# Kernel tuning notes

Measured on AMD Instinct MI355X. Metric: run time of the kernel, lower is better.

The kernel has to match this reference:

```python
import jax, jax.numpy as jnp
import numpy as np

LN_EPS = 1e-5


def layernorm(x, g, b):
    mu = jnp.mean(x, axis=-1, keepdims=True)
    var = jnp.mean((x - mu) ** 2, axis=-1, keepdims=True)
    return (x - mu) * jax.lax.rsqrt(var + LN_EPS) * g + b


def attention(x, qkv_w, proj_w, proj_b, num_heads):
    B, N, C = x.shape
    d = C // num_heads
    qkv = jnp.einsum('bnc,oc->bno', x, qkv_w)            # [B,N,3C], no bias (qkv_bias=False)
    qkv = qkv.reshape(B, N, num_heads, 3 * d).transpose(0, 2, 1, 3)  # [B,h,N,3d]
    q, k, v = qkv[..., :d], qkv[..., d:2 * d], qkv[..., 2 * d:]
    scores = jnp.einsum('bhnd,bhmd->bhnm', q, k) * (d ** -0.5)
    a = jax.nn.softmax(scores, axis=-1)
    o = jnp.einsum('bhnm,bhmd->bhnd', a, v).transpose(0, 2, 1, 3).reshape(B, N, C)
    return jnp.einsum('bnc,oc->bno', o, proj_w) + proj_b


def dwconv(x, w, b, H, W):
    # x: [B,N,C] -> NCHW depthwise 3x3 conv, stride 1, pad 1 -> [B,N,C]
    B, N, C = x.shape
    xi = x.transpose(0, 2, 1).reshape(B, C, H, W)
    y = jax.lax.conv_general_dilated(
        xi, w, window_strides=(1, 1), padding='SAME',
        dimension_numbers=('NCHW', 'OIHW', 'NCHW'), feature_group_count=C)
    y = y + b[None, :, None, None]
    return y.reshape(B, C, H * W).transpose(0, 2, 1)


def mlp(x, fc1_w, fc1_b, dw_w, dw_b, fc2_w, fc2_b, H, W):
    h = jnp.einsum('bnc,oc->bno', x, fc1_w) + fc1_b
    h = dwconv(h, dw_w, dw_b, H, W)
    h = jax.nn.gelu(h, approximate=False)  # torch nn.GELU default = exact erf
    return jnp.einsum('bnh,oh->bno', h, fc2_w) + fc2_b


def setup_inputs() -> dict:
    key = jax.random.key(0)
    ks = jax.random.split(key, 8)
    B, N, C, HID = 8, 1024, 512, 2048
    s = 0.02
    return {
        'x': jax.random.normal(ks[0], (B, N, C), jnp.float32),
        'ln1_g': jnp.ones((C,), jnp.float32),
        'ln1_b': jnp.zeros((C,), jnp.float32),
        'qkv_w': jax.random.normal(ks[1], (3 * C, C), jnp.float32) * s,
        'proj_w': jax.random.normal(ks[2], (C, C), jnp.float32) * s,
        'proj_b': jnp.zeros((C,), jnp.float32),
        'ln2_g': jnp.ones((C,), jnp.float32),
        'ln2_b': jnp.zeros((C,), jnp.float32),
        'fc1_w': jax.random.normal(ks[3], (HID, C), jnp.float32) * s,
        'fc1_b': jnp.zeros((HID,), jnp.float32),
        'dw_w': jax.random.normal(ks[4], (HID, 1, 3, 3), jnp.float32) * s,
        'dw_b': jnp.zeros((HID,), jnp.float32),
        'fc2_w': jax.random.normal(ks[5], (C, HID), jnp.float32) * s,
        'fc2_b': jnp.zeros((C,), jnp.float32),
        'H': 32,
        'W': 32,
    }


def reference(x, ln1_g, ln1_b, qkv_w, proj_w, proj_b, ln2_g, ln2_b,
              fc1_w, fc1_b, dw_w, dw_b, fc2_w, fc2_b, H, W):
    NUM_HEADS = 8
    x = x + attention(layernorm(x, ln1_g, ln1_b), qkv_w, proj_w, proj_b, NUM_HEADS)
    x = x + mlp(layernorm(x, ln2_g, ln2_b), fc1_w, fc1_b, dw_w, dw_b, fc2_w, fc2_b, H, W)
    return x
```

## Files before the change

### kernel.cpp

```cpp
#include <hip/hip_runtime.h>
#include <hip/hip_bf16.h>


typedef __attribute__((ext_vector_type(8))) short short8;
typedef __attribute__((ext_vector_type(4))) short s16x4;
typedef __attribute__((ext_vector_type(4))) float f32x4;

__device__ __forceinline__ float b2f(short s) {
    union { float f; unsigned u; } z; z.u = ((unsigned)(unsigned short)s) << 16; return z.f;
}
__device__ __forceinline__ short f2b(float f) {
    union { float f; unsigned u; } z; z.f = f;
    unsigned r = (z.u + 0x7fffu + ((z.u >> 16) & 1u)) >> 16;
    return (short)r;
}
__device__ __forceinline__ float erf_fast(float x) {
    float ax = fabsf(x);
    float t = 1.0f / fmaf(0.3275911f, ax, 1.0f);
    float p = t * fmaf(t, fmaf(t, fmaf(t, fmaf(t, 1.061405429f, -1.453152027f),
                        1.421413741f), -0.284496736f), 0.254829592f);
    float r = 1.0f - p * __expf(-ax * ax);
    return x < 0.f ? -r : r;
}

__device__ __forceinline__ void gload_lds16(const void* g, void* l) {
    __builtin_amdgcn_global_load_lds(
        (const __attribute__((address_space(1))) void*)g,
        (__attribute__((address_space(3))) void*)l, 16, 0, 0);
}

__global__ __launch_bounds__(256) void cvt_weights(
    const float* __restrict__ s0, const float* __restrict__ s1,
    const float* __restrict__ s2, const float* __restrict__ s3,
    short* __restrict__ d0, short* __restrict__ d1,
    short* __restrict__ d2, short* __restrict__ d3) {
    long i = (long)blockIdx.x * 256 + threadIdx.x;
    const float* s; short* d; long off;
    if (i < 196608)      { s = s0; d = d0; off = i; }
    else if (i < 262144) { s = s1; d = d1; off = i - 196608; }
    else if (i < 524288) { s = s2; d = d2; off = i - 262144; }
    else                 { s = s3; d = d3; off = i - 524288; }
    float4 v = ((const float4*)s)[off];
    ushort4 o;
    o.x = (unsigned short)f2b(v.x); o.y = (unsigned short)f2b(v.y);
    o.z = (unsigned short)f2b(v.z); o.w = (unsigned short)f2b(v.w);
    ((ushort4*)d)[off] = o;
}

__global__ __launch_bounds__(256) void cvt_dw(
    const float* __restrict__ src, float* __restrict__ dst) {
    int i = blockIdx.x * 256 + threadIdx.x;
    int t = i >> 11, c = i & 2047;
    dst[t * 2048 + c] = src[c * 9 + t];
}

__global__ __launch_bounds__(256) void ln_kernel(
    const float* __restrict__ x, const float* __restrict__ g,
    const float* __restrict__ b, short* __restrict__ y) {
    int row  = blockIdx.x * 4 + (threadIdx.x >> 6);
    int lane = threadIdx.x & 63;
    const float* xr = x + (long)row * 512 + lane * 8;
    float4 v0 = ((const float4*)xr)[0];
    float4 v1 = ((const float4*)xr)[1];
    float e0[8] = {v0.x, v0.y, v0.z, v0.w, v1.x, v1.y, v1.z, v1.w};
    float s = 0.f;
#pragma unroll
    for (int e = 0; e < 8; e++) s += e0[e];
#pragma unroll
    for (int d = 1; d < 64; d <<= 1) s += __shfl_xor(s, d);
    float mu = s * (1.0f / 512.0f);
    float q = 0.f;
#pragma unroll
    for (int e = 0; e < 8; e++) { float t = e0[e] - mu; q += t * t; }
#pragma unroll
    for (int d = 1; d < 64; d <<= 1) q += __shfl_xor(q, d);
    float rs = rsqrtf(q * (1.0f / 512.0f) + 1e-5f);
    const float* gp = g + lane * 8;
    const float* bp = b + lane * 8;
    short8 o;
#pragma unroll
    for (int e = 0; e < 8; e++) o[e] = f2b((e0[e] - mu) * rs * gp[e] + bp[e]);
    *(short8*)(y + (long)row * 512 + lane * 8) = o;
}

template <int MT, typename Epi>
__global__ __launch_bounds__(256, 4) void gemm_bt(
    const short* __restrict__ A, const short* __restrict__ B, int K, Epi epi) {
    constexpr int NJ = (MT == 128) ? 4 : 2;
    __shared__ short As[MT * 64];
    __shared__ short Bs[128 * 64];
    int tid = threadIdx.x;
    int lane = tid & 63, w = tid >> 6;
    int lr = lane & 15, lq = lane >> 4;
    int wm = (MT == 128) ? (w & 1) * 64 : 0;
    int wn = (MT == 128) ? (w >> 1) * 64 : w * 32;
    long r0 = (long)blockIdx.x * MT, o0 = (long)blockIdx.y * 128;
    f32x4 acc[4][NJ];
#pragma unroll
    for (int i = 0; i < 4; i++)
#pragma unroll
        for (int j = 0; j < NJ; j++) acc[i][j] = (f32x4){0.f, 0.f, 0.f, 0.f};
    const short* Ab = A + r0 * K;
    const short* Bb = B + o0 * K;
    int srow = tid >> 3;
    int sc = ((tid & 7) ^ (srow & 7)) * 8;
    for (int k0 = 0; k0 < K; k0 += 64) {
#pragma unroll
        for (int m = 0; m < MT / 32; m++)
            gload_lds16(Ab + (long)(srow + m * 32) * K + k0 + sc,
                        As + m * 2048 + w * 512);
#pragma unroll
        for (int m = 0; m < 4; m++)
            gload_lds16(Bb + (long)(srow + m * 32) * K + k0 + sc,
                        Bs + m * 2048 + w * 512);
        __syncthreads();
#pragma unroll
        for (int ks = 0; ks < 2; ks++) {
            short8 af[4], bfr[NJ];
#pragma unroll
            for (int i = 0; i < 4; i++) {
                int row = wm + i * 16 + lr;
                int c = ks * 4 + lq;
                af[i] = *(const short8*)&As[row * 64 + ((c ^ (row & 7)) * 8)];
            }
#pragma unroll
            for (int j = 0; j < NJ; j++) {
                int row = wn + j * 16 + lr;
                int c = ks * 4 + lq;
                bfr[j] = *(const short8*)&Bs[row * 64 + ((c ^ (row & 7)) * 8)];
            }
#pragma unroll
            for (int i = 0; i < 4; i++)
#pragma unroll
                for (int j = 0; j < NJ; j++)
                    acc[i][j] = __builtin_amdgcn_mfma_f32_16x16x32_bf16(
                        af[i], bfr[j], acc[i][j], 0, 0, 0);
        }
        __syncthreads();
    }
#pragma unroll
    for (int i = 0; i < 4; i++)
#pragma unroll
        for (int j = 0; j < NJ; j++)
#pragma unroll
            for (int rg = 0; rg < 4; rg++)
                epi((int)(r0 + wm + i * 16 + lq * 4 + rg),
                    (int)(o0 + wn + j * 16 + lr), acc[i][j][rg]);
}

struct EpiQKV {
    short *q, *k, *vt;
    __device__ void operator()(int r, int o, float v) const {
        int b = r >> 10, n = r & 1023;
        int h = o / 192, j = o - h * 192;
        int bh = b * 8 + h;
        short bv = f2b(v);
        if (j < 64)        q[((long)bh * 1024 + n) * 64 + j] = bv;
        else if (j < 128)  k[((long)bh * 1024 + n) * 64 + (j - 64)] = bv;
        else               vt[((long)bh * 64 + (j - 128)) * 1024 + n] = bv;
    }
};
struct EpiProj {
    const float* pb; const float* x; float* x1;
    __device__ void operator()(int r, int o, float v) const {
        long idx = (long)r * 512 + o;
        x1[idx] = v + pb[o] + x[idx];
    }
};
struct EpiBias {
    const float* bias; short* out; int O;
    __device__ void operator()(int r, int o, float v) const {
        out[(long)r * O + o] = f2b(v + bias[o]);
    }
};
struct EpiFc2 {
    const float* bias; const float* x1; float* out;
    __device__ void operator()(int r, int o, float v) const {
        long idx = (long)r * 512 + o;
        out[idx] = v + bias[o] + x1[idx];
    }
};

__global__ __launch_bounds__(256, 3) void attn_kernel(
    const short* __restrict__ Q, const short* __restrict__ K,
    const short* __restrict__ Vt, short* __restrict__ out) {
    __shared__ __align__(16) char smem[53248];
    int bh = blockIdx.x, qb = blockIdx.y;
    int tid = threadIdx.x, w = tid >> 6, lane = tid & 63;
    int lr = lane & 15, lq = lane >> 4;
    short* Kt = (short*)(smem + w * 13312);
    short* Vl = (short*)(smem + w * 13312 + 4096);
    short* Pt = (short*)(smem + w * 13312 + 8192);
    short* Oshb = (short*)smem;
    float* Lsh  = (float*)(smem + 36864);

    const short* Qb = Q + ((long)bh * 1024 + qb * 64) * 64;
    const short* Kb = K + (long)bh * 1024 * 64;
    const short* Vb = Vt + (long)bh * 64 * 1024;

    short8 qf[4][2];
#pragma unroll
    for (int jt = 0; jt < 4; jt++)
#pragma unroll
        for (int ks = 0; ks < 2; ks++)
            qf[jt][ks] = *(const short8*)(Qb + (jt * 16 + lr) * 64 + ks * 32 + lq * 8);

    f32x4 oacc[4][4];
#pragma unroll
    for (int mt = 0; mt < 4; mt++)
#pragma unroll
        for (int dt = 0; dt < 4; dt++) oacc[mt][dt] = (f32x4){0.f, 0.f, 0.f, 0.f};
    float lsum[4] = {0.f, 0.f, 0.f, 0.f};

    for (int it = 0; it < 8; it++) {
        int n0 = w * 256 + it * 32;
#pragma unroll
        for (int i = 0; i < 4; i++) {
            int s = i * 64 + lane;
            int row = s >> 3, ch = (s & 7) ^ (row & 7);
            gload_lds16(Kb + (long)(n0 + row) * 64 + ch * 8, Kt + i * 512);
        }
#pragma unroll
        for (int i = 0; i < 4; i++) {
            int s = i * 64 + lane;
            int row = s >> 2, ch = s & 3;
            gload_lds16(Vb + (long)row * 1024 + n0 + ch * 8, Vl + i * 512);
        }
        asm volatile("s_waitcnt vmcnt(0)" ::: "memory");
        f32x4 sacc[2][4];
#pragma unroll
        for (int kt = 0; kt < 2; kt++)
#pragma unroll
            for (int jt = 0; jt < 4; jt++) sacc[kt][jt] = (f32x4){0.f, 0.f, 0.f, 0.f};
#pragma unroll
        for (int ks = 0; ks < 2; ks++)
#pragma unroll
            for (int kt = 0; kt < 2; kt++) {
                short8 ak = *(const short8*)&Kt[(kt * 16 + lr) * 64 +
                                                (((ks * 4 + lq) ^ (lr & 7)) * 8)];
#pragma unroll
                for (int jt = 0; jt < 4; jt++)
                    sacc[kt][jt] = __builtin_amdgcn_mfma_f32_16x16x32_bf16(
                        ak, qf[jt][ks], sacc[kt][jt], 0, 0, 0);
            }
#pragma unroll
        for (int kt = 0; kt < 2; kt++)
#pragma unroll
            for (int jt = 0; jt < 4; jt++) {
                float e0 = __expf(sacc[kt][jt][0] * 0.125f);
                float e1 = __expf(sacc[kt][jt][1] * 0.125f);
                float e2 = __expf(sacc[kt][jt][2] * 0.125f);
                float e3 = __expf(sacc[kt][jt][3] * 0.125f);
                lsum[jt] += (e0 + e1) + (e2 + e3);
                uint2 pk;
                pk.x = (__float_as_uint(e1) & 0xffff0000u) | (__float_as_uint(e0) >> 16);
                pk.y = (__float_as_uint(e3) & 0xffff0000u) | (__float_as_uint(e2) >> 16);
                *(uint2*)&Pt[(jt * 16 + lr) * 36 + kt * 16 + lq * 4] = pk;
            }
        short8 bv[4];
#pragma unroll
        for (int dt = 0; dt < 4; dt++)
            bv[dt] = *(const short8*)&Vl[(dt * 16 + lr) * 32 + lq * 8];
#pragma unroll
        for (int mt = 0; mt < 4; mt++) {
            short8 ap = *(const short8*)&Pt[(mt * 16 + lr) * 36 + lq * 8];
#pragma unroll
            for (int dt = 0; dt < 4; dt++)
                oacc[mt][dt] = __builtin_amdgcn_mfma_f32_16x16x32_bf16(
                    ap, bv[dt], oacc[mt][dt], 0, 0, 0);
        }
    }
#pragma unroll
    for (int jt = 0; jt < 4; jt++) {
        lsum[jt] += __shfl_xor(lsum[jt], 16);
        lsum[jt] += __shfl_xor(lsum[jt], 32);
    }
    __syncthreads();
#pragma unroll
    for (int mt = 0; mt < 4; mt++)
#pragma unroll
        for (int dt = 0; dt < 4; dt++)
#pragma unroll
            for (int rg = 0; rg < 4; rg++)
                Oshb[w * 4608 + (mt * 16 + lq * 4 + rg) * 72 + dt * 16 + lr] =
                    f2b(oacc[mt][dt][rg]);
    if (lq == 0)
#pragma unroll
        for (int jt = 0; jt < 4; jt++) Lsh[w * 64 + jt * 16 + lr] = lsum[jt];
    __syncthreads();
    int m = tid >> 2, dg = (tid & 3) * 16;
    float l = Lsh[m] + Lsh[64 + m] + Lsh[128 + m] + Lsh[192 + m];
    float inv = 1.0f / l;
    float r[16];
#pragma unroll
    for (int i = 0; i < 16; i++) r[i] = 0.f;
#pragma unroll
    for (int ww = 0; ww < 4; ww++) {
        const short8* op = (const short8*)&Oshb[ww * 4608 + m * 72 + dg];
        short8 a = op[0], bq = op[1];
#pragma unroll
        for (int i = 0; i < 8; i++) { r[i] += b2f(a[i]); r[8 + i] += b2f(bq[i]); }
    }
    short8 o0, o1;
#pragma unroll
    for (int i = 0; i < 8; i++) { o0[i] = f2b(r[i] * inv); o1[i] = f2b(r[8 + i] * inv); }
    int b = bh >> 3, h = bh & 7;
    long base = ((long)(b * 1024 + qb * 64 + m)) * 512 + h * 64 + dg;
    *(short8*)(out + base) = o0;
    *(short8*)(out + base + 8) = o1;
}

__global__ __launch_bounds__(256, 3) void dwconv_gelu(
    const short* __restrict__ h1, const float* __restrict__ wdT,
    const float* __restrict__ bias, short* __restrict__ h2) {
    int ch = blockIdx.x & 1, xq = (blockIdx.x >> 1) & 3;
    int yy = (blockIdx.x >> 3) & 31, b = blockIdx.x >> 8;
    int c0 = ch * 1024 + threadIdx.x * 4;
    int x0 = xq * 8;
    float w[9][4];
#pragma unroll
    for (int t = 0; t < 9; t++) {
        float4 v = *(const float4*)&wdT[t * 2048 + c0];
        w[t][0] = v.x; w[t][1] = v.y; w[t][2] = v.z; w[t][3] = v.w;
    }
    float4 bv = *(const float4*)&bias[c0];
    float acc[8][4];
#pragma unroll
    for (int xi = 0; xi < 8; xi++) {
        acc[xi][0] = bv.x; acc[xi][1] = bv.y; acc[xi][2] = bv.z; acc[xi][3] = bv.w;
    }
#pragma unroll
    for (int ky = 0; ky < 3; ky++) {
        int ys = yy + ky - 1;
        if (ys < 0 || ys > 31) continue;
        const short* rp = h1 + ((long)(b * 1024 + ys * 32) * 2048 + c0);
        float fa[4], fb[4], fc[4];
        if (x0 > 0) {
            s16x4 v = *(const s16x4*)(rp + (long)(x0 - 1) * 2048);
#pragma unroll
            for (int e = 0; e < 4; e++) fa[e] = b2f(v[e]);
        } else {
#pragma unroll
            for (int e = 0; e < 4; e++) fa[e] = 0.f;
        }
        {
            s16x4 v = *(const s16x4*)(rp + (long)x0 * 2048);
#pragma unroll
            for (int e = 0; e < 4; e++) fb[e] = b2f(v[e]);
        }
#pragma unroll
        for (int xi = 0; xi < 8; xi++) {
            int xs = x0 + xi + 1;
            if (xs <= 31) {
                s16x4 v = *(const s16x4*)(rp + (long)xs * 2048);
#pragma unroll
                for (int e = 0; e < 4; e++) fc[e] = b2f(v[e]);
            } else {
#pragma unroll
                for (int e = 0; e < 4; e++) fc[e] = 0.f;
            }
#pragma unroll
            for (int e = 0; e < 4; e++)
                acc[xi][e] += fa[e] * w[ky * 3][e] + fb[e] * w[ky * 3 + 1][e] +
                              fc[e] * w[ky * 3 + 2][e];
#pragma unroll
            for (int e = 0; e < 4; e++) { fa[e] = fb[e]; fb[e] = fc[e]; }
        }
    }
#pragma unroll
    for (int xi = 0; xi < 8; xi++) {
        s16x4 o;
#pragma unroll
        for (int e = 0; e < 4; e++) {
            float a = acc[xi][e];
            o[e] = f2b(0.5f * a * (1.0f + erf_fast(a * 0.70710678118f)));
        }
        *(s16x4*)&h2[(long)(b * 1024 + yy * 32 + x0 + xi) * 2048 + c0] = o;
    }
}

extern "C" void kernel_launch(void* const* d_in, const int* in_sizes, int n_in,
                              void* d_out, int out_size, void* d_ws, size_t ws_size,
                              hipStream_t stream) {
    const float* x      = (const float*)d_in[0];
    const float* ln1_g  = (const float*)d_in[1];
    const float* ln1_b  = (const float*)d_in[2];
    const float* qkv_w  = (const float*)d_in[3];
    const float* proj_w = (const float*)d_in[4];
    const float* proj_b = (const float*)d_in[5];
    const float* ln2_g  = (const float*)d_in[6];
    const float* ln2_b  = (const float*)d_in[7];
    const float* fc1_w  = (const float*)d_in[8];
    const float* fc1_b  = (const float*)d_in[9];
    const float* dw_w   = (const float*)d_in[10];
    const float* dw_b   = (const float*)d_in[11];
    const float* fc2_w  = (const float*)d_in[12];
    const float* fc2_b  = (const float*)d_in[13];
    float* out = (float*)d_out;

    char* p = (char*)d_ws;
    short* wq   = (short*)p; p += (long)1536 * 512 * 2;
    short* wp   = (short*)p; p += (long)512 * 512 * 2;
    short* w1   = (short*)p; p += (long)2048 * 512 * 2;
    short* w2   = (short*)p; p += (long)512 * 2048 * 2;
    float* wdT  = (float*)p; p += (long)9 * 2048 * 4;
    short* y1   = (short*)p; p += (long)8192 * 512 * 2;
    short* q    = (short*)p; p += (long)64 * 1024 * 64 * 2;
    short* k    = (short*)p; p += (long)64 * 1024 * 64 * 2;
    short* vt   = (short*)p; p += (long)64 * 64 * 1024 * 2;
    short* attn = (short*)p; p += (long)8192 * 512 * 2;
    float* x1   = (float*)p; p += (long)8192 * 512 * 4;
    short* y2   = (short*)p; p += (long)8192 * 512 * 2;
    short* h1   = (short*)p; p += (long)8192 * 2048 * 2;
    short* h2   = (short*)p; p += (long)8192 * 2048 * 2;
    if ((size_t)(p - (char*)d_ws) > ws_size) return;

    cvt_weights<<<3072, 256, 0, stream>>>(qkv_w, proj_w, fc1_w, fc2_w, wq, wp, w1, w2);
    cvt_dw<<<72, 256, 0, stream>>>(dw_w, wdT);
    ln_kernel<<<2048, 256, 0, stream>>>(x, ln1_g, ln1_b, y1);
    gemm_bt<128><<<dim3(64, 12), 256, 0, stream>>>(y1, wq, 512, EpiQKV{q, k, vt});
    attn_kernel<<<dim3(64, 16), 256, 0, stream>>>(q, k, vt, attn);
    gemm_bt<64><<<dim3(128, 4), 256, 0, stream>>>(attn, wp, 512,
                                                  EpiProj{proj_b, x, x1});
    ln_kernel<<<2048, 256, 0, stream>>>(x1, ln2_g, ln2_b, y2);
    gemm_bt<128><<<dim3(64, 16), 256, 0, stream>>>(y2, w1, 512,
                                                   EpiBias{fc1_b, h1, 2048});
    dwconv_gelu<<<2048, 256, 0, stream>>>(h1, wdT, dw_b, h2);
    gemm_bt<64><<<dim3(128, 4), 256, 0, stream>>>(h2, w2, 2048,
                                                  EpiFc2{fc2_b, x1, out});
}
```

Before: 274.4 us.

## Split attention across query rows per wave with shared double-buffered K/V tiles

The attention kernel used to give each wave a slice of the key range for all 64 queries and then reduced the four partial outputs through shared memory. Now each wave owns 16 query rows and walks the full key range. The four waves share one double-buffered K/V tile that is loaded cooperatively and prefetched one step ahead under a block barrier. This removes the cross-wave reduction and its bf16 round trip, cuts shared memory so more blocks can fit per CU, and swaps expf for exp2f with a folded scale. In exchange it adds a __syncthreads every iteration and writes the output with scalar 2-byte stores instead of vector stores.

```diff
diff --git a/kernel.cpp b/kernel.cpp
--- a/kernel.cpp
+++ b/kernel.cpp
@@ -181,133 +181,108 @@
     }
 };
 
-__global__ __launch_bounds__(256, 3) void attn_kernel(
+__global__ __launch_bounds__(256, 4) void attn_kernel(
     const short* __restrict__ Q, const short* __restrict__ K,
     const short* __restrict__ Vt, short* __restrict__ out) {
-    __shared__ __align__(16) char smem[53248];
+    __shared__ __align__(16) char smem[40960];
     int bh = blockIdx.x, qb = blockIdx.y;
     int tid = threadIdx.x, w = tid >> 6, lane = tid & 63;
     int lr = lane & 15, lq = lane >> 4;
-    short* Kt = (short*)(smem + w * 13312);
-    short* Vl = (short*)(smem + w * 13312 + 4096);
-    short* Pt = (short*)(smem + w * 13312 + 8192);
-    short* Oshb = (short*)smem;
-    float* Lsh  = (float*)(smem + 36864);
-
-    const short* Qb = Q + ((long)bh * 1024 + qb * 64) * 64;
+    short* Pt = (short*)(smem + 32768) + w * 1024;
+
+    const short* Qb = Q + ((long)bh * 1024 + qb * 64 + w * 16) * 64;
     const short* Kb = K + (long)bh * 1024 * 64;
     const short* Vb = Vt + (long)bh * 64 * 1024;
 
-    short8 qf[4][2];
-#pragma unroll
-    for (int jt = 0; jt < 4; jt++)
+    int srow8 = lane >> 3, slot = lane & 7;
+
+    short8 qf[2];
+    qf[0] = *(const short8*)(Qb + lr * 64 + lq * 8);
+    qf[1] = *(const short8*)(Qb + lr * 64 + 32 + lq * 8);
+
+    f32x4 oacc[4];
+#pragma unroll
+    for (int dt = 0; dt < 4; dt++) oacc[dt] = (f32x4){0.f, 0.f, 0.f, 0.f};
+    float lsum = 0.f;
+
+#pragma unroll
+    for (int m = 0; m < 2; m++) {
+        int row = m * 32 + w * 8 + srow8;
+        gload_lds16(Kb + (long)row * 64 + ((slot ^ (row & 7)) * 8),
+                    (short*)smem + (m * 32 + w * 8) * 64);
+        gload_lds16(Vb + (long)row * 1024 + ((slot ^ (row & 7)) * 8),
+                    (short*)(smem + 16384) + (m * 32 + w * 8) * 64);
+    }
+
+    for (int it = 0; it < 16; it++) {
+        __syncthreads();
+        int cb = (it & 1) * 8192;
+        if (it + 1 < 16) {
+            int n0 = (it + 1) * 64, nb = ((it + 1) & 1) * 8192;
+#pragma unroll
+            for (int m = 0; m < 2; m++) {
+                int row = m * 32 + w * 8 + srow8;
+                gload_lds16(Kb + (long)(n0 + row) * 64 + ((slot ^ (row & 7)) * 8),
+                            (short*)(smem + nb) + (m * 32 + w * 8) * 64);
+                gload_lds16(Vb + (long)row * 1024 + n0 + ((slot ^ (row & 7)) * 8),
+                            (short*)(smem + 16384 + nb) + (m * 32 + w * 8) * 64);
+            }
+        }
+        const short* Kt = (const short*)(smem + cb);
+        const short* Vl = (const short*)(smem + 16384 + cb);
+        f32x4 sacc[4];
+#pragma unroll
+        for (int kt = 0; kt < 4; kt++) sacc[kt] = (f32x4){0.f, 0.f, 0.f, 0.f};
 #pragma unroll
         for (int ks = 0; ks < 2; ks++)
-            qf[jt][ks] = *(const short8*)(Qb + (jt * 16 + lr) * 64 + ks * 32 + lq * 8);
-
-    f32x4 oacc[4][4];
-#pragma unroll
-    for (int mt = 0; mt < 4; mt++)
-#pragma unroll
-        for (int dt = 0; dt < 4; dt++) oacc[mt][dt] = (f32x4){0.f, 0.f, 0.f, 0.f};
-    float lsum[4] = {0.f, 0.f, 0.f, 0.f};
-
-    for (int it = 0; it < 8; it++) {
-        int n0 = w * 256 + it * 32;
-#pragma unroll
-        for (int i = 0; i < 4; i++) {
-            int s = i * 64 + lane;
-            int row = s >> 3, ch = (s & 7) ^ (row & 7);
-            gload_lds16(Kb + (long)(n0 + row) * 64 + ch * 8, Kt + i * 512);
-        }
-#pragma unroll
-        for (int i = 0; i < 4; i++) {
-            int s = i * 64 + lane;
-            int row = s >> 2, ch = s & 3;
-            gload_lds16(Vb + (long)row * 1024 + n0 + ch * 8, Vl + i * 512);
-        }
-        asm volatile("s_waitcnt vmcnt(0)" ::: "memory");
-        f32x4 sacc[2][4];
-#pragma unroll
-        for (int kt = 0; kt < 2; kt++)
-#pragma unroll
-            for (int jt = 0; jt < 4; jt++) sacc[kt][jt] = (f32x4){0.f, 0.f, 0.f, 0.f};
-#pragma unroll
-        for (int ks = 0; ks < 2; ks++)
-#pragma unroll
-            for (int kt = 0; kt < 2; kt++) {
-                short8 ak = *(const short8*)&Kt[(kt * 16 + lr) * 64 +
-                                                (((ks * 4 + lq) ^ (lr & 7)) * 8)];
-#pragma unroll
-                for (int jt = 0; jt < 4; jt++)
-                    sacc[kt][jt] = __builtin_amdgcn_mfma_f32_16x16x32_bf16(
-                        ak, qf[jt][ks], sacc[kt][jt], 0, 0, 0);
-            }
-#pragma unroll
-        for (int kt = 0; kt < 2; kt++)
-#pragma unroll
-            for (int jt = 0; jt < 4; jt++) {
-                float e0 = __expf(sacc[kt][jt][0] * 0.125f);
-                float e1 = __expf(sacc[kt][jt][1] * 0.125f);
-                float e2 = __expf(sacc[kt][jt][2] * 0.125f);
-                float e3 = __expf(sacc[kt][jt][3] * 0.125f);
-                lsum[jt] += (e0 + e1) + (e2 + e3);
-                uint2 pk;
-                pk.x = (__float_as_uint(e1) & 0xffff0000u) | (__float_as_uint(e0) >> 16);
-                pk.y = (__float_as_uint(e3) & 0xffff0000u) | (__float_as_uint(e2) >> 16);
-                *(uint2*)&Pt[(jt * 16 + lr) * 36 + kt * 16 + lq * 4] = pk;
-            }
-        short8 bv[4];
+#pragma unroll
+            for (int kt = 0; kt < 4; kt++) {
+                int row = kt * 16 + lr;
+                short8 ak = *(const short8*)&Kt[row * 64 +
+                                                (((ks * 4 + lq) ^ (row & 7)) * 8)];
+                sacc[kt] = __builtin_amdgcn_mfma_f32_16x16x32_bf16(
+                    ak, qf[ks], sacc[kt], 0, 0, 0);
+            }
+#pragma unroll
+        for (int kt = 0; kt < 4; kt++) {
+            float e0 = exp2f(sacc[kt][0] * 0.18033688f);
+            float e1 = exp2f(sacc[kt][1] * 0.18033688f);
+            float e2 = exp2f(sacc[kt][2] * 0.18033688f);
+            float e3 = exp2f(sacc[kt][3] * 0.18033688f);
+            lsum += (e0 + e1) + (e2 + e3);
+            uint2 pk;
+            pk.x = (__float_as_uint(e1) & 0xffff0000u) | (__float_as_uint(e0) >> 16);
+            pk.y = (__float_as_uint(e3) & 0xffff0000u) | (__float_as_uint(e2) >> 16);
+            int chunk = kt * 2 + (lq >> 1);
+            *(uint2*)&Pt[lr * 64 + ((chunk ^ (lr & 7)) * 8) + (lq & 1) * 4] = pk;
+        }
+#pragma unroll
+        for (int ks = 0; ks < 2; ks++) {
+            short8 ap = *(const short8*)&Pt[lr * 64 +
+                                            (((ks * 4 + lq) ^ (lr & 7)) * 8)];
+#pragma unroll
+            for (int dt = 0; dt < 4; dt++) {
+                int row = dt * 16 + lr;
+                short8 bv = *(const short8*)&Vl[row * 64 +
+                                                (((ks * 4 + lq) ^ (row & 7)) * 8)];
+                oacc[dt] = __builtin_amdgcn_mfma_f32_16x16x32_bf16(
+                    ap, bv, oacc[dt], 0, 0, 0);
+            }
+        }
+    }
+    lsum += __shfl_xor(lsum, 16);
+    lsum += __shfl_xor(lsum, 32);
+    float inv = 1.0f / lsum;
+    int b = bh >> 3, h = bh & 7;
+    int qbase = qb * 64 + w * 16;
+#pragma unroll
+    for (int rg = 0; rg < 4; rg++) {
+        float iv = __shfl(inv, lq * 4 + rg);
+        long base = ((long)(b * 1024 + qbase + lq * 4 + rg)) * 512 + h * 64;
 #pragma unroll
         for (int dt = 0; dt < 4; dt++)
-            bv[dt] = *(const short8*)&Vl[(dt * 16 + lr) * 32 + lq * 8];
-#pragma unroll
-        for (int mt = 0; mt < 4; mt++) {
-            short8 ap = *(const short8*)&Pt[(mt * 16 + lr) * 36 + lq * 8];
-#pragma unroll
-            for (int dt = 0; dt < 4; dt++)
-                oacc[mt][dt] = __builtin_amdgcn_mfma_f32_16x16x32_bf16(
-                    ap, bv[dt], oacc[mt][dt], 0, 0, 0);
-        }
-    }
-#pragma unroll
-    for (int jt = 0; jt < 4; jt++) {
-        lsum[jt] += __shfl_xor(lsum[jt], 16);
-        lsum[jt] += __shfl_xor(lsum[jt], 32);
-    }
-    __syncthreads();
-#pragma unroll
-    for (int mt = 0; mt < 4; mt++)
-#pragma unroll
-        for (int dt = 0; dt < 4; dt++)
-#pragma unroll
-            for (int rg = 0; rg < 4; rg++)
-                Oshb[w * 4608 + (mt * 16 + lq * 4 + rg) * 72 + dt * 16 + lr] =
-                    f2b(oacc[mt][dt][rg]);
-    if (lq == 0)
-#pragma unroll
-        for (int jt = 0; jt < 4; jt++) Lsh[w * 64 + jt * 16 + lr] = lsum[jt];
-    __syncthreads();
-    int m = tid >> 2, dg = (tid & 3) * 16;
-    float l = Lsh[m] + Lsh[64 + m] + Lsh[128 + m] + Lsh[192 + m];
-    float inv = 1.0f / l;
-    float r[16];
-#pragma unroll
-    for (int i = 0; i < 16; i++) r[i] = 0.f;
-#pragma unroll
-    for (int ww = 0; ww < 4; ww++) {
-        const short8* op = (const short8*)&Oshb[ww * 4608 + m * 72 + dg];
-        short8 a = op[0], bq = op[1];
-#pragma unroll
-        for (int i = 0; i < 8; i++) { r[i] += b2f(a[i]); r[8 + i] += b2f(bq[i]); }
-    }
-    short8 o0, o1;
-#pragma unroll
-    for (int i = 0; i < 8; i++) { o0[i] = f2b(r[i] * inv); o1[i] = f2b(r[8 + i] * inv); }
-    int b = bh >> 3, h = bh & 7;
-    long base = ((long)(b * 1024 + qb * 64 + m)) * 512 + h * 64 + dg;
-    *(short8*)(out + base) = o0;
-    *(short8*)(out + base + 8) = o1;
+            out[base + dt * 16 + lr] = f2b(oacc[dt][rg] * iv);
+    }
 }
 
 __global__ __launch_bounds__(256, 3) void dwconv_gelu(
```

Result: no change. 271.5 us (-1.1%).
